# Kernel optimization log

Hardware: AMD Instinct MI355X
Metric: run time of the kernel (lower is better)

The kernel has to match this reference:

```python
import jax, jax.numpy as jnp
import numpy as np

D = 256          # d_model
NH = 8           # heads
NP = 4           # points per level
NL = 4           # feature levels
DH = D // NH     # head dim = 32
MLP = 4 * D      # 1024
B = 2
SHAPES = [(128, 128), (64, 64), (32, 32), (16, 16)]
LQ = sum(h * w for h, w in SHAPES)  # 21760
EPS = 1e-6


def layer_norm(x, g, b):
    mu = jnp.mean(x, axis=-1, keepdims=True)
    var = jnp.mean(jnp.square(x - mu), axis=-1, keepdims=True)
    return (x - mu) * jax.lax.rsqrt(var + EPS) * g + b


def bilinear_sample(val_l, loc, Hs, Ws):
    # val_l: [B, Hs*Ws, NH, DH]; loc: [B, Lq, NH, NP, 2] normalized in [0,1]
    v = val_l.transpose(0, 2, 1, 3)                      # [B, NH, HW, DH]
    x = loc[..., 0] * Ws - 0.5                           # [B, Lq, NH, NP]
    y = loc[..., 1] * Hs - 0.5
    x0 = jnp.floor(x); y0 = jnp.floor(y)
    lx = x - x0; ly = y - y0
    x0i = x0.astype(jnp.int32); y0i = y0.astype(jnp.int32)

    def gather(xi, yi):
        inb = (xi >= 0) & (xi < Ws) & (yi >= 0) & (yi < Hs)
        idx = jnp.clip(yi, 0, Hs - 1) * Ws + jnp.clip(xi, 0, Ws - 1)
        idx = idx.transpose(0, 2, 1, 3)                  # [B, NH, Lq, NP]
        sh = idx.shape
        idxf = idx.reshape(sh[0], sh[1], -1)
        g = jax.vmap(jax.vmap(lambda vv, ii: vv[ii]))(v, idxf)
        g = g.reshape(sh[0], sh[1], sh[2], sh[3], v.shape[-1])
        return g * inb.transpose(0, 2, 1, 3)[..., None].astype(g.dtype)

    wt = lambda a: a.transpose(0, 2, 1, 3)[..., None]    # -> [B, NH, Lq, NP, 1]
    out = (gather(x0i, y0i) * wt((1 - lx) * (1 - ly))
           + gather(x0i + 1, y0i) * wt(lx * (1 - ly))
           + gather(x0i, y0i + 1) * wt((1 - lx) * ly)
           + gather(x0i + 1, y0i + 1) * wt(lx * ly))
    return out                                            # [B, NH, Lq, NP, DH]


def setup_inputs() -> dict:
    key = jax.random.key(0)
    ks = jax.random.split(key, 16)
    ss = np.array(SHAPES, dtype=np.int64)
    lsi = np.concatenate([[0], np.cumsum(ss[:, 0] * ss[:, 1])[:-1]]).astype(np.int64)
    s = 0.02
    return {
        'src': jax.random.normal(ks[0], (B, LQ, D), jnp.float32),
        'pos': jax.random.normal(ks[1], (B, LQ, D), jnp.float32),
        'reference_points': jax.random.uniform(ks[2], (B, LQ, NL, 2), jnp.float32),
        'spatial_shapes': ss,
        'level_start_index': lsi,
        'g1': jnp.ones((D,), jnp.float32), 'beta1': jnp.zeros((D,), jnp.float32),
        'w_off': jax.random.normal(ks[3], (D, NH * NL * NP * 2), jnp.float32) * 0.01,
        'b_off': jax.random.normal(ks[4], (NH * NL * NP * 2,), jnp.float32) * 0.1,
        'w_attn': jax.random.normal(ks[5], (D, NH * NL * NP), jnp.float32) * s,
        'b_attn': jnp.zeros((NH * NL * NP,), jnp.float32),
        'w_val': jax.random.normal(ks[6], (D, D), jnp.float32) * s,
        'b_val': jnp.zeros((D,), jnp.float32),
        'w_out': jax.random.normal(ks[7], (D, D), jnp.float32) * s,
        'b_out': jnp.zeros((D,), jnp.float32),
        'g2': jnp.ones((D,), jnp.float32), 'beta2': jnp.zeros((D,), jnp.float32),
        'w_fc1': jax.random.normal(ks[8], (D, MLP), jnp.float32) * s,
        'b_fc1': jnp.zeros((MLP,), jnp.float32),
        'w_fc2': jax.random.normal(ks[9], (MLP, D), jnp.float32) * s,
        'b_fc2': jnp.zeros((D,), jnp.float32),
    }


def reference(src, pos, reference_points, spatial_shapes, level_start_index,
              g1, beta1, w_off, b_off, w_attn, b_attn, w_val, b_val,
              w_out, b_out, g2, beta2, w_fc1, b_fc1, w_fc2, b_fc2):
    ss = np.asarray(spatial_shapes)
    lsi = np.asarray(level_start_index)
    Bsz, Lq, _ = src.shape

    # --- pre-norm + multi-scale deformable attention + residual ---
    x = layer_norm(src, g1, beta1)
    q = x + pos
    val = (x @ w_val + b_val).reshape(Bsz, Lq, NH, DH)
    off = (q @ w_off + b_off).reshape(Bsz, Lq, NH, NL, NP, 2)
    aw = jax.nn.softmax((q @ w_attn + b_attn).reshape(Bsz, Lq, NH, NL * NP), axis=-1)
    aw = aw.reshape(Bsz, Lq, NH, NL, NP)

    out = jnp.zeros((Bsz, Lq, NH, DH), src.dtype)
    for l in range(NL):
        Hs, Ws = int(ss[l, 0]), int(ss[l, 1])
        start = int(lsi[l])
        vl = val[:, start:start + Hs * Ws]                       # [B, HW, NH, DH]
        norm = jnp.array([Ws, Hs], src.dtype)
        loc = reference_points[:, :, None, l, None, :] + off[:, :, :, l] / norm
        samp = bilinear_sample(vl, loc, Hs, Ws)                  # [B, NH, Lq, NP, DH]
        a = aw[:, :, :, l].transpose(0, 2, 1, 3)                 # [B, NH, Lq, NP]
        out = out + jnp.einsum('bhqp,bhqpd->bqhd', a, samp)
    attn_out = out.reshape(Bsz, Lq, D) @ w_out + b_out
    src2 = src + attn_out

    # --- pre-norm MLP + residual ---
    y = layer_norm(src2, g2, beta2)
    ffn = jax.nn.relu(y @ w_fc1 + b_fc1) @ w_fc2 + b_fc2
    return src2 + ffn
```

## Files before the change

### kernel.cpp

```cpp
#include <hip/hip_runtime.h>

#define DMODEL 256
#define NHEAD 8
#define NPOINT 4
#define NLEVEL 4
#define DHEAD 32
#define MLPD 1024
#define BSZ 2
#define LQTOK 21760
#define NTOK (BSZ * LQTOK)
#define LNEPS 1e-6f

typedef __attribute__((ext_vector_type(8))) short short8;
typedef __attribute__((ext_vector_type(4))) float f32x4;
typedef __attribute__((ext_vector_type(2))) float f32x2;

__device__ __forceinline__ float bf2f(unsigned short u) {
  unsigned int i = ((unsigned int)u) << 16;
  return __builtin_bit_cast(float, i);
}
__device__ __forceinline__ unsigned short f2bf(float f) {
  unsigned int i = __builtin_bit_cast(unsigned int, f);
  i += 0x7fff + ((i >> 16) & 1);
  return (unsigned short)(i >> 16);
}
__device__ __forceinline__ float bflo(unsigned int u) {
  return __builtin_bit_cast(float, u << 16);
}
__device__ __forceinline__ float bfhi(unsigned int u) {
  return __builtin_bit_cast(float, u & 0xffff0000u);
}

__device__ __forceinline__ void pk_fma_bcast(f32x2& d, f32x2 a, float b) {
  f32x2 bb;
  bb[0] = b;
  bb[1] = b;
  asm("v_pk_fma_f32 %0, %1, %2, %0" : "+v"(d) : "v"(a), "v"(bb));
}

__device__ __forceinline__ void gload_lds16(const unsigned short* g,
                                            unsigned short* lds) {
  __builtin_amdgcn_global_load_lds(
      (const __attribute__((address_space(1))) unsigned int*)g,
      (__attribute__((address_space(3))) unsigned int*)lds, 16, 0, 0);
}

template <bool EMITQ>
__global__ __launch_bounds__(256) void ln_bf16(
    const float* __restrict__ in, const float* __restrict__ g,
    const float* __restrict__ beta, unsigned short* __restrict__ o,
    const float* __restrict__ pos, unsigned short* __restrict__ q) {
  const int w = threadIdx.x >> 6, lane = threadIdx.x & 63;
  const size_t t = (size_t)blockIdx.x * 4 + w;
  const size_t base = t * DMODEL + lane * 4;
  float4 v = *(const float4*)(in + base);
  float s = (v.x + v.y) + (v.z + v.w);
#pragma unroll
  for (int off = 32; off; off >>= 1) s += __shfl_xor(s, off, 64);
  float mu = s * (1.0f / DMODEL);
  float dx = v.x - mu, dy = v.y - mu, dz = v.z - mu, dw = v.w - mu;
  float s2 = (dx * dx + dy * dy) + (dz * dz + dw * dw);
#pragma unroll
  for (int off = 32; off; off >>= 1) s2 += __shfl_xor(s2, off, 64);
  float rs = rsqrtf(s2 * (1.0f / DMODEL) + LNEPS);
  float4 gg = *(const float4*)(g + lane * 4);
  float4 bb = *(const float4*)(beta + lane * 4);
  unsigned short r0 = f2bf(dx * rs * gg.x + bb.x);
  unsigned short r1 = f2bf(dy * rs * gg.y + bb.y);
  unsigned short r2 = f2bf(dz * rs * gg.z + bb.z);
  unsigned short r3 = f2bf(dw * rs * gg.w + bb.w);
  unsigned int lo = ((unsigned int)r1 << 16) | r0;
  unsigned int hi = ((unsigned int)r3 << 16) | r2;
  *(uint2*)(o + base) = make_uint2(lo, hi);
  if (EMITQ) {
    float4 p = *(const float4*)(pos + base);
    unsigned short q0 = f2bf(bf2f(r0) + p.x);
    unsigned short q1 = f2bf(bf2f(r1) + p.y);
    unsigned short q2 = f2bf(bf2f(r2) + p.z);
    unsigned short q3 = f2bf(bf2f(r3) + p.w);
    unsigned int ql = ((unsigned int)q1 << 16) | q0;
    unsigned int qh = ((unsigned int)q3 << 16) | q2;
    *(uint2*)(q + base) = make_uint2(ql, qh);
  }
}

__global__ __launch_bounds__(256) void transpose_bf16(const float* __restrict__ W,
                                                      unsigned short* __restrict__ Wt,
                                                      int K, int N) {
  __shared__ float tile[32][33];
  int k0 = blockIdx.x * 32, n0 = blockIdx.y * 32;
  int tx = threadIdx.x & 31, ty = threadIdx.x >> 5;
  for (int i = ty; i < 32; i += 8) tile[i][tx] = W[(size_t)(k0 + i) * N + n0 + tx];
  __syncthreads();
  for (int i = ty; i < 32; i += 8)
    Wt[(size_t)(n0 + i) * K + k0 + tx] = f2bf(tile[tx][i]);
}

template <int OMODE>
__global__ __launch_bounds__(256) void gemm_mfma(
    const unsigned short* __restrict__ A, const unsigned short* __restrict__ Wt,
    const float* __restrict__ bias, const float* __restrict__ res,
    void* __restrict__ Cout, void* __restrict__ Cout2, int M, int N, int K) {
  __shared__ __attribute__((aligned(16))) unsigned short As[128 * 32];
  __shared__ __attribute__((aligned(16))) unsigned short Bs[128 * 32];
  const int tid = threadIdx.x;
  const int m0 = blockIdx.x * 128, n0 = blockIdx.y * 128;
  const int wave = tid >> 6, lane = tid & 63;
  const int wm = (wave & 1) * 64, wn = (wave >> 1) * 64;
  const int lr = lane & 15, quad = lane >> 4;
  f32x4 acc[4][4] = {};
  for (int k0 = 0; k0 < K; k0 += 32) {
    __syncthreads();
#pragma unroll
    for (int r = 0; r < 2; r++) {
      int c = r * 256 + tid;
      int row = c >> 2, col8 = (c & 3) * 8;
      gload_lds16(Wt + (size_t)(n0 + row) * K + k0 + col8,
                  &Bs[(r * 256 + wave * 64) * 8]);
    }
#pragma unroll
    for (int r = 0; r < 2; r++) {
      int c = r * 256 + tid;
      int row = c >> 2, col8 = (c & 3) * 8;
      gload_lds16(A + (size_t)(m0 + row) * K + k0 + col8,
                  &As[(r * 256 + wave * 64) * 8]);
    }
    __syncthreads();
    short8 af[4], bfr[4];
#pragma unroll
    for (int i = 0; i < 4; i++)
      af[i] = *(const short8*)(&As[(wm + i * 16 + lr) * 32 + quad * 8]);
#pragma unroll
    for (int j = 0; j < 4; j++)
      bfr[j] = *(const short8*)(&Bs[(wn + j * 16 + lr) * 32 + quad * 8]);
#pragma unroll
    for (int i = 0; i < 4; i++)
#pragma unroll
      for (int j = 0; j < 4; j++)
        acc[i][j] = __builtin_amdgcn_mfma_f32_16x16x32_bf16(af[i], bfr[j],
                                                            acc[i][j], 0, 0, 0);
  }
#pragma unroll
  for (int i = 0; i < 4; i++) {
    int rbase = m0 + wm + i * 16 + quad * 4;
#pragma unroll
    for (int j = 0; j < 4; j++) {
      int col = n0 + wn + j * 16 + lr;
      float bv = (OMODE == 4 && col >= 256) ? res[col - 256] : bias[col];
#pragma unroll
      for (int r = 0; r < 4; r++) {
        float v = acc[i][j][r] + bv;
        if (OMODE == 2) v = fmaxf(v, 0.0f);
        if (OMODE == 4) {
          size_t row = (size_t)(rbase + r);
          if (col < 256)
            ((unsigned short*)Cout)[row * 256 + col] = f2bf(v);
          else
            ((unsigned short*)Cout2)[row * 128 + (col - 256)] = f2bf(v);
        } else {
          size_t idx = (size_t)(rbase + r) * N + col;
          if (OMODE == 3) {
            ((float*)Cout)[idx] = v + res[idx];
          } else {
            ((unsigned short*)Cout)[idx] = f2bf(v);
          }
        }
      }
    }
  }
}

__global__ __launch_bounds__(256) void deform_sample(
    const unsigned short* __restrict__ val, const unsigned short* __restrict__ off,
    const unsigned short* __restrict__ logits, const float* __restrict__ refp,
    unsigned short* __restrict__ out) {
  __shared__ __attribute__((aligned(16))) int sIdx[4][16][8][4];
  __shared__ __attribute__((aligned(16))) float sW[4][16][8][4];
  const int w = threadIdx.x >> 6, lane = threadIdx.x & 63;
  const int bq = blockIdx.x * 4 + w;
  const int b = __builtin_amdgcn_readfirstlane(bq / LQTOK);
  {
    const int HW_[4] = {128, 64, 32, 16};
    const int LSI_[4] = {0, 16384, 20480, 21504};
    int u0 = 2 * lane;
    int h = u0 >> 4;
    int lvl = (u0 >> 2) & 3;
    int pt0 = u0 & 15;
    int HW = HW_[lvl];
    float2 rp = ((const float2*)refp)[(size_t)bq * 4 + lvl];
    uint2 ov = *(const uint2*)(off + (size_t)bq * 256 + 4 * lane);
    unsigned int lgu = *(const unsigned int*)(logits + (size_t)bq * 128 + 2 * lane);
    float lg0 = bflo(lgu), lg1 = bfhi(lgu);
    float mx = fmaxf(lg0, lg1);
#pragma unroll
    for (int s = 1; s < 8; s <<= 1) mx = fmaxf(mx, __shfl_xor(mx, s, 64));
    float e0 = expf(lg0 - mx), e1 = expf(lg1 - mx);
    float es = e0 + e1;
#pragma unroll
    for (int s = 1; s < 8; s <<= 1) es += __shfl_xor(es, s, 64);
    float inv = 1.0f / es;
    float a01[2] = {e0 * inv, e1 * inv};
    unsigned int ovv[2] = {ov.x, ov.y};
    int hb2 = h * (DHEAD * 2);
#pragma unroll
    for (int c = 0; c < 2; c++) {
      float x = fmaf(rp.x, (float)HW, bflo(ovv[c])) - 0.5f;
      float y = fmaf(rp.y, (float)HW, bfhi(ovv[c])) - 0.5f;
      float xf = floorf(x), yf = floorf(y);
      int x0 = (int)xf, y0 = (int)yf;
      float lx = x - xf, ly = y - yf;
      int x0c = min(max(x0, 0), HW - 1);
      int x1c = min(max(x0 + 1, 0), HW - 1);
      int y0c = min(max(y0, 0), HW - 1);
      int y1c = min(max(y0 + 1, 0), HW - 1);
      float m0x = (x0 >= 0 && x0 < HW) ? 1.f : 0.f;
      float m1x = (x0 + 1 >= 0 && x0 + 1 < HW) ? 1.f : 0.f;
      float m0y = (y0 >= 0 && y0 < HW) ? 1.f : 0.f;
      float m1y = (y0 + 1 >= 0 && y0 + 1 < HW) ? 1.f : 0.f;
      float a = a01[c];
      int pt = pt0 + c;
      int hs = h ^ (pt & 7);
      int r0 = (LSI_[lvl] + y0c * HW) * (DMODEL * 2) + hb2;
      int r1 = (LSI_[lvl] + y1c * HW) * (DMODEL * 2) + hb2;
      *(int4*)sIdx[w][pt][hs] =
          make_int4(r0 + x0c * (DMODEL * 2), r0 + x1c * (DMODEL * 2),
                    r1 + x0c * (DMODEL * 2), r1 + x1c * (DMODEL * 2));
      *(float4*)sW[w][pt][hs] =
          make_float4((1.f - lx) * (1.f - ly) * m0x * m0y * a,
                      lx * (1.f - ly) * m1x * m0y * a,
                      (1.f - lx) * ly * m0x * m1y * a,
                      lx * ly * m1x * m1y * a);
    }
  }
  __builtin_amdgcn_wave_barrier();
  const int h2 = lane >> 3, g = lane & 7;
  const char* basep =
      (const char*)val + (size_t)b * ((size_t)LQTOK * DMODEL * 2);
  const int goff = g * 8;
  f32x2 a01v = {0.f, 0.f}, a23v = {0.f, 0.f};
#pragma unroll
  for (int pb = 0; pb < 4; pb++) {
    int4 ix[4];
    float4 wt4[4];
#pragma unroll
    for (int p = 0; p < 4; p++) {
      int pt = pb * 4 + p;
      int hs = h2 ^ (pt & 7);
      ix[p] = *(const int4*)sIdx[w][pt][hs];
      wt4[p] = *(const float4*)sW[w][pt][hs];
    }
    uint2 v4[4][4];
#pragma unroll
    for (int p = 0; p < 4; p++) {
      v4[p][0] = *(const uint2*)(basep + (unsigned)(ix[p].x + goff));
      v4[p][1] = *(const uint2*)(basep + (unsigned)(ix[p].y + goff));
      v4[p][2] = *(const uint2*)(basep + (unsigned)(ix[p].z + goff));
      v4[p][3] = *(const uint2*)(basep + (unsigned)(ix[p].w + goff));
    }
#pragma unroll
    for (int p = 0; p < 4; p++) {
      float wk[4] = {wt4[p].x, wt4[p].y, wt4[p].z, wt4[p].w};
#pragma unroll
      for (int k = 0; k < 4; k++) {
        uint2 u = v4[p][k];
        f32x2 vlo, vhi;
        vlo[0] = bflo(u.x);
        vlo[1] = bfhi(u.x);
        vhi[0] = bflo(u.y);
        vhi[1] = bfhi(u.y);
        pk_fma_bcast(a01v, vlo, wk[k]);
        pk_fma_bcast(a23v, vhi, wk[k]);
      }
    }
  }
  unsigned int o0 = ((unsigned int)f2bf(a01v[1]) << 16) | f2bf(a01v[0]);
  unsigned int o1 = ((unsigned int)f2bf(a23v[1]) << 16) | f2bf(a23v[0]);
  *(uint2*)(out + (size_t)bq * 256 + h2 * 32 + g * 4) = make_uint2(o0, o1);
}

extern "C" void kernel_launch(void* const* d_in, const int* in_sizes, int n_in,
                              void* d_out, int out_size, void* d_ws,
                              size_t ws_size, hipStream_t stream) {
  const float* src    = (const float*)d_in[0];
  const float* pos    = (const float*)d_in[1];
  const float* refp   = (const float*)d_in[2];
  const float* g1     = (const float*)d_in[5];
  const float* beta1  = (const float*)d_in[6];
  const float* w_off  = (const float*)d_in[7];
  const float* b_off  = (const float*)d_in[8];
  const float* w_attn = (const float*)d_in[9];
  const float* b_attn = (const float*)d_in[10];
  const float* w_val  = (const float*)d_in[11];
  const float* b_val  = (const float*)d_in[12];
  const float* w_out  = (const float*)d_in[13];
  const float* b_out  = (const float*)d_in[14];
  const float* g2     = (const float*)d_in[15];
  const float* beta2  = (const float*)d_in[16];
  const float* w_fc1  = (const float*)d_in[17];
  const float* b_fc1  = (const float*)d_in[18];
  const float* w_fc2  = (const float*)d_in[19];
  const float* b_fc2  = (const float*)d_in[20];
  float* out = (float*)d_out;

  const size_t NT = (size_t)NTOK;
  unsigned short* b1 = (unsigned short*)d_ws;
  unsigned short* b2 = b1 + NT * 256;
  unsigned short* b3 = b2 + NT * 256;
  unsigned short* b4 = b3 + NT * 256;
  unsigned short* b5 = b4 + NT * 256;
  unsigned short* wvalT  = b5 + NT * 512;
  unsigned short* woffaT = wvalT + 256 * 256;
  unsigned short* woutT  = woffaT + 384 * 256;
  unsigned short* wfc1T  = woutT + 256 * 256;
  unsigned short* wfc2T  = wfc1T + 1024 * 256;

  unsigned short* qb  = b4;
  unsigned short* lgb = b5;
  unsigned short* yb  = b5;
  unsigned short* hid = b1;

  transpose_bf16<<<dim3(8, 8), 256, 0, stream>>>(w_val, wvalT, 256, 256);
  transpose_bf16<<<dim3(8, 8), 256, 0, stream>>>(w_off, woffaT, 256, 256);
  transpose_bf16<<<dim3(8, 4), 256, 0, stream>>>(w_attn, woffaT + 256 * 256,
                                                 256, 128);
  transpose_bf16<<<dim3(8, 8), 256, 0, stream>>>(w_out, woutT, 256, 256);
  transpose_bf16<<<dim3(8, 32), 256, 0, stream>>>(w_fc1, wfc1T, 256, 1024);
  transpose_bf16<<<dim3(32, 8), 256, 0, stream>>>(w_fc2, wfc2T, 1024, 256);

  const int MT = NTOK / 128;

  ln_bf16<true><<<NTOK / 4, 256, 0, stream>>>(src, g1, beta1, b1, pos, qb);
  gemm_mfma<1><<<dim3(MT, 2), 256, 0, stream>>>(b1, wvalT, b_val, nullptr, b2,
                                                nullptr, NTOK, 256, 256);
  gemm_mfma<4><<<dim3(MT, 3), 256, 0, stream>>>(qb, woffaT, b_off, b_attn, b3,
                                                lgb, NTOK, 384, 256);
  deform_sample<<<NTOK / 4, 256, 0, stream>>>(b2, b3, lgb, refp, b1);
  gemm_mfma<3><<<dim3(MT, 2), 256, 0, stream>>>(b1, woutT, b_out, src, out,
                                                nullptr, NTOK, 256, 256);
  ln_bf16<false><<<NTOK / 4, 256, 0, stream>>>(out, g2, beta2, yb, nullptr,
                                               nullptr);
  gemm_mfma<2><<<dim3(MT, 8), 256, 0, stream>>>(yb, wfc1T, b_fc1, nullptr, hid,
                                                nullptr, NTOK, 1024, 256);
  gemm_mfma<3><<<dim3(MT, 2), 256, 0, stream>>>(hid, wfc2T, b_fc2, out, out,
                                                nullptr, NTOK, 256, 1024);
}
```

Baseline: 445.8 us.

## Remap GEMM workgroups per XCD and use op_sel broadcast in sampling FMAs

The GEMM kernel now remaps its linear workgroup id so that consecutive tiles land on the same XCD, which should improve L2 reuse of shared A/B tiles across the chiplets. Separately, the deformable sampling loop stops building broadcast weight pairs and instead uses v_pk_fma_f32 op_sel/op_sel_hi modifiers to read the low or high weight lane directly, removing the register moves. The remap adds a few integer divisions per block, and the inline asm depends on op_sel semantics being correct for packed fp32.

```diff
diff --git a/kernel.cpp b/kernel.cpp
--- a/kernel.cpp
+++ b/kernel.cpp
@@ -31,11 +31,15 @@
   return __builtin_bit_cast(float, u & 0xffff0000u);
 }
 
-__device__ __forceinline__ void pk_fma_bcast(f32x2& d, f32x2 a, float b) {
-  f32x2 bb;
-  bb[0] = b;
-  bb[1] = b;
-  asm("v_pk_fma_f32 %0, %1, %2, %0" : "+v"(d) : "v"(a), "v"(bb));
+__device__ __forceinline__ void pk_fma_blo(f32x2& d, f32x2 a, f32x2 b) {
+  asm("v_pk_fma_f32 %0, %1, %2, %0 op_sel:[0,0,0] op_sel_hi:[1,0,1]"
+      : "+v"(d)
+      : "v"(a), "v"(b));
+}
+__device__ __forceinline__ void pk_fma_bhi(f32x2& d, f32x2 a, f32x2 b) {
+  asm("v_pk_fma_f32 %0, %1, %2, %0 op_sel:[0,1,0] op_sel_hi:[1,1,1]"
+      : "+v"(d)
+      : "v"(a), "v"(b));
 }
 
 __device__ __forceinline__ void gload_lds16(const unsigned short* g,
@@ -104,7 +108,15 @@
   __shared__ __attribute__((aligned(16))) unsigned short As[128 * 32];
   __shared__ __attribute__((aligned(16))) unsigned short Bs[128 * 32];
   const int tid = threadIdx.x;
-  const int m0 = blockIdx.x * 128, n0 = blockIdx.y * 128;
+  const unsigned gx = gridDim.x, gy = gridDim.y;
+  const unsigned nwg = gx * gy;
+  const unsigned orig = blockIdx.y * gx + blockIdx.x;
+  const unsigned xcd = orig & 7u, rest = orig >> 3;
+  const unsigned qq = nwg >> 3, rr = nwg & 7u;
+  const unsigned wgid =
+      (xcd < rr ? xcd * (qq + 1) : rr * (qq + 1) + (xcd - rr) * qq) + rest;
+  const int m0 = (int)(wgid / gy) * 128;
+  const int n0 = (int)(wgid % gy) * 128;
   const int wave = tid >> 6, lane = tid & 63;
   const int wm = (wave & 1) * 64, wn = (wave >> 1) * 64;
   const int lr = lane & 15, quad = lane >> 4;
@@ -241,13 +253,13 @@
 #pragma unroll
   for (int pb = 0; pb < 4; pb++) {
     int4 ix[4];
-    float4 wt4[4];
+    f32x4 wt4[4];
 #pragma unroll
     for (int p = 0; p < 4; p++) {
       int pt = pb * 4 + p;
       int hs = h2 ^ (pt & 7);
       ix[p] = *(const int4*)sIdx[w][pt][hs];
-      wt4[p] = *(const float4*)sW[w][pt][hs];
+      wt4[p] = *(const f32x4*)sW[w][pt][hs];
     }
     uint2 v4[4][4];
 #pragma unroll
@@ -259,7 +271,8 @@
     }
 #pragma unroll
     for (int p = 0; p < 4; p++) {
-      float wk[4] = {wt4[p].x, wt4[p].y, wt4[p].z, wt4[p].w};
+      f32x2 w01 = __builtin_shufflevector(wt4[p], wt4[p], 0, 1);
+      f32x2 w23 = __builtin_shufflevector(wt4[p], wt4[p], 2, 3);
 #pragma unroll
       for (int k = 0; k < 4; k++) {
         uint2 u = v4[p][k];
@@ -268,8 +281,14 @@
         vlo[1] = bfhi(u.x);
         vhi[0] = bflo(u.y);
         vhi[1] = bfhi(u.y);
-        pk_fma_bcast(a01v, vlo, wk[k]);
-        pk_fma_bcast(a23v, vhi, wk[k]);
+        f32x2 wp = (k < 2) ? w01 : w23;
+        if ((k & 1) == 0) {
+          pk_fma_blo(a01v, vlo, wp);
+          pk_fma_blo(a23v, vhi, wp);
+        } else {
+          pk_fma_bhi(a01v, vlo, wp);
+          pk_fma_bhi(a23v, vhi, wp);
+        }
       }
     }
   }
```

Result: no change. 437.8 us (-1.8%).
